# Kernel optimization log

Hardware: AMD Instinct MI355X
Metric: run time of the kernel (lower is better)

Reference implementation:

```python
import jax, jax.numpy as jnp
import numpy as np

B, C, O, H, W, K, PAD = 8, 256, 256, 56, 56, 3, 1
KK = K * K


def setup_inputs() -> dict:
    key = jax.random.key(0)
    k1, k2, k3, k4 = jax.random.split(key, 4)
    x = jax.random.normal(k1, (B, C, H, W), jnp.float32)
    # offset conv params (original zero-inits; small random used so sampling is off-grid)
    w_off = jax.random.normal(k2, (2 * KK, C, K, K), jnp.float32) * 0.01
    b_off = jnp.zeros((2 * KK,), jnp.float32)
    # deformable conv weight/bias (torchvision DeformConv2d default has bias)
    w_dcn = jax.random.normal(k3, (O, C, K, K), jnp.float32) * (1.0 / np.sqrt(C * KK))
    b_dcn = jax.random.normal(k4, (O,), jnp.float32) * 0.01
    return dict(x=x, w_off=w_off, b_off=b_off, w_dcn=w_dcn, b_dcn=b_dcn)


def _conv3x3(x, w, b):
    y = jax.lax.conv_general_dilated(
        x, w, window_strides=(1, 1), padding=((PAD, PAD), (PAD, PAD)),
        dimension_numbers=('NCHW', 'OIHW', 'NCHW'))
    return y + b[None, :, None, None]


def _deform_sample(x, py, px):
    """Zero-padded bilinear gather of x[B,C,H,W] at (py,px)[B,KK,H,W] -> [B,C,KK,H,W]."""
    xf = x.reshape(B, C, H * W)
    y0 = jnp.floor(py)
    x0 = jnp.floor(px)
    fy = py - y0
    fx = px - x0
    val = 0.0
    for dy, dx, wgt in ((0, 0, (1 - fy) * (1 - fx)),
                        (0, 1, (1 - fy) * fx),
                        (1, 0, fy * (1 - fx)),
                        (1, 1, fy * fx)):
        yc = y0 + dy
        xc = x0 + dx
        ok = (yc >= 0) & (yc < H) & (xc >= 0) & (xc < W)  # zero-padding outside
        yi = jnp.clip(yc, 0, H - 1).astype(jnp.int32)
        xi = jnp.clip(xc, 0, W - 1).astype(jnp.int32)
        idx = (yi * W + xi).reshape(B, 1, KK * H * W)  # broadcast over channel dim
        g = jnp.take_along_axis(xf, idx, axis=2).reshape(B, C, KK, H, W)
        val = val + (wgt * ok)[:, None] * g
    return val


def reference(x, w_off, b_off, w_dcn, b_dcn):
    # 1) predict per-pixel offsets: [B, 2*K*K, H, W], torchvision layout (dy,dx) pairs
    off = _conv3x3(x, w_off, b_off)
    dy = off[:, 0::2]  # [B, KK, H, W]
    dx = off[:, 1::2]
    # 2) sampling grid: base pixel + kernel tap offset + learned offset
    ky = (jnp.arange(KK) // K - PAD).astype(jnp.float32)
    kx = (jnp.arange(KK) % K - PAD).astype(jnp.float32)
    hgrid = jnp.arange(H, dtype=jnp.float32)
    wgrid = jnp.arange(W, dtype=jnp.float32)
    py = hgrid[None, None, :, None] + ky[None, :, None, None] + dy
    px = wgrid[None, None, None, :] + kx[None, :, None, None] + dx
    # 3) bilinear gather + weighted accumulation over (c, kernel tap)
    val = _deform_sample(x, py, px)  # [B, C, KK, H, W]
    out = jnp.einsum('bckhw,ock->bohw', val, w_dcn.reshape(O, C, KK))
    return out + b_dcn[None, :, None, None]
```

## Files before the change

### kernel.cpp

```cpp
#include <hip/hip_runtime.h>

#define B_  8
#define C_  256
#define O_  256
#define H_  56
#define W_  56
#define HW_ 3136
#define KK_ 9
#define CK_ 2304
#define NKC 72

typedef __bf16    bf16x8 __attribute__((ext_vector_type(8)));
typedef float     f32x4  __attribute__((ext_vector_type(4)));

__device__ __forceinline__ int swz4(int r) { return (r & 3) ^ ((r >> 2) & 3); }

__device__ __forceinline__ float blo(unsigned u) {
    return __builtin_bit_cast(float, u << 16);
}
__device__ __forceinline__ float bhi(unsigned u) {
    return __builtin_bit_cast(float, u & 0xffff0000u);
}
__device__ __forceinline__ unsigned pkbf(float lo, float hi) {
    unsigned short a = __builtin_bit_cast(unsigned short, (__bf16)lo);
    unsigned short b = __builtin_bit_cast(unsigned short, (__bf16)hi);
    return (unsigned)a | ((unsigned)b << 16);
}

__device__ __forceinline__ uint4 bilin4(uint4 c00, uint4 c01, uint4 c10, uint4 c11,
                                        float4 wg) {
    uint4 o;
    float lo_, hi_;
    lo_ = wg.x*blo(c00.x) + wg.y*blo(c01.x) + wg.z*blo(c10.x) + wg.w*blo(c11.x);
    hi_ = wg.x*bhi(c00.x) + wg.y*bhi(c01.x) + wg.z*bhi(c10.x) + wg.w*bhi(c11.x);
    o.x = pkbf(lo_, hi_);
    lo_ = wg.x*blo(c00.y) + wg.y*blo(c01.y) + wg.z*blo(c10.y) + wg.w*blo(c11.y);
    hi_ = wg.x*bhi(c00.y) + wg.y*bhi(c01.y) + wg.z*bhi(c10.y) + wg.w*bhi(c11.y);
    o.y = pkbf(lo_, hi_);
    lo_ = wg.x*blo(c00.z) + wg.y*blo(c01.z) + wg.z*blo(c10.z) + wg.w*blo(c11.z);
    hi_ = wg.x*bhi(c00.z) + wg.y*bhi(c01.z) + wg.z*bhi(c10.z) + wg.w*bhi(c11.z);
    o.z = pkbf(lo_, hi_);
    lo_ = wg.x*blo(c00.w) + wg.y*blo(c01.w) + wg.z*blo(c10.w) + wg.w*blo(c11.w);
    hi_ = wg.x*bhi(c00.w) + wg.y*bhi(c01.w) + wg.z*bhi(c10.w) + wg.w*bhi(c11.w);
    o.w = pkbf(lo_, hi_);
    return o;
}

__global__ __launch_bounds__(256) void k_buildA(const float* __restrict__ w,
                                                unsigned short* __restrict__ wA) {
    int d  = blockIdx.x * 256 + threadIdx.x;
    int kc = d >> 13;
    int rd = d & 8191;
    int m  = rd >> 5;
    int pos = rd & 31;
    int q  = (pos >> 3) ^ swz4(m);
    int kl = q * 8 + (pos & 7);
    int gk = kc * 32 + kl;
    int tap = gk >> 8, c = gk & 255;
    __bf16 v = (__bf16)w[m * CK_ + c * KK_ + tap];
    wA[d] = __builtin_bit_cast(unsigned short, v);
}

__global__ __launch_bounds__(256) void k_transx(const float* __restrict__ x,
                                                unsigned short* __restrict__ xT) {
    __shared__ float s[64][65];
    int bt   = blockIdx.x;
    int c64  = bt & 3;
    int hw64 = (bt >> 2) % 49;
    int b    = bt / 196;
    int tx = threadIdx.x & 63;
    int ty = threadIdx.x >> 6;
#pragma unroll
    for (int i = 0; i < 16; ++i)
        s[i * 4 + ty][tx] =
            x[((size_t)(b * 256 + c64 * 64 + i * 4 + ty)) * HW_ + hw64 * 64 + tx];
    __syncthreads();
#pragma unroll
    for (int i = 0; i < 16; ++i) {
        float v = s[tx][i * 4 + ty];
        xT[((size_t)b * HW_ + hw64 * 64 + i * 4 + ty) * 256 + c64 * 64 + tx] =
            __builtin_bit_cast(unsigned short, (__bf16)v);
    }
}

__global__ __launch_bounds__(512) void k_offc1(const float* __restrict__ x,
                                               const float* __restrict__ w_off,
                                               float* __restrict__ part) {
    __shared__ float partial[8][64][18];
    int t  = threadIdx.x;
    int p  = t & 63;
    int cg = __builtin_amdgcn_readfirstlane(t >> 6);
    int orig = blockIdx.x;
    int blk  = (orig & 7) * 196 + (orig >> 3);
    int sl   = blk & 3;
    int un   = blk >> 2;
    int b    = un / 49;
    int pos0 = (un % 49) * 64;
    int pos  = pos0 + p;
    int h = pos / W_;
    int w = pos % W_;
    const float* xb = x + (size_t)b * C_ * HW_;

    float acc[18];
#pragma unroll
    for (int i = 0; i < 18; ++i) acc[i] = 0.f;

    for (int cc = 0; cc < 8; ++cc) {
        int c = sl * 64 + cg * 8 + cc;
        const float* xp = xb + c * HW_;
        float v[9];
#pragma unroll
        for (int dh = -1; dh <= 1; ++dh)
#pragma unroll
            for (int dw = -1; dw <= 1; ++dw) {
                int hh = h + dh, ww = w + dw;
                bool ok = (hh >= 0) & (hh < H_) & (ww >= 0) & (ww < W_);
                v[(dh + 1) * 3 + dw + 1] = ok ? xp[hh * W_ + ww] : 0.f;
            }
        const float* wc = w_off + c * KK_;
#pragma unroll
        for (int oc = 0; oc < 18; ++oc) {
            const float* wr = wc + oc * CK_;
#pragma unroll
            for (int k = 0; k < KK_; ++k)
                acc[oc] = fmaf(v[k], wr[k], acc[oc]);
        }
    }
#pragma unroll
    for (int oc = 0; oc < 18; ++oc) partial[cg][p][oc] = acc[oc];
    __syncthreads();

    float* po = part + (size_t)sl * (B_ * 18 * HW_);
    for (int e = t; e < 64 * 18; e += 512) {
        int oc = e >> 6;
        int pp = e & 63;
        float s = 0.f;
#pragma unroll
        for (int g = 0; g < 8; ++g) s += partial[g][pp][oc];
        po[((size_t)b * 18 + oc) * HW_ + pos0 + pp] = s;
    }
}

__global__ __launch_bounds__(256) void k_offc2(const float* __restrict__ part,
                                               const float* __restrict__ b_off,
                                               float* __restrict__ off) {
    int i = blockIdx.x * 256 + threadIdx.x;
    const int NP = B_ * 18 * HW_;
    int oc = (i / HW_) % 18;
    off[i] = part[i] + part[i + NP] + part[i + 2 * NP] + part[i + 3 * NP]
           + b_off[oc];
}

template<bool ISSUEC, bool ISSUEA, bool PROD, bool RELID, bool RELWG>
__device__ __forceinline__ void fstage(
    int s, int chNext,
    const char* xb, const char* gA0,
    __bf16 (*s_b)[2048],
    int (*s_id)[64][4], float (*s_w)[64][4],
    int4& id, float4& wg,
    uint4 (&cUse)[4], uint4 (&cFill)[4],
    bf16x8 (&afUse)[4], bf16x8 (&afFill)[4],
    int aoffBase,
    int n, int tc, int sc, int lid, int quad, int swz,
    f32x4 (&acc)[4][4]) {

    if (RELID) {
        id = *(const int4*)s_id[(s + 2) >> 3][n];
    }
    if (RELWG) {
        wg = *(const float4*)s_w[(s + 1) >> 3][n];
    }
    if (ISSUEC) {
        const char* p = xb + chNext * 64 + tc * 16;
        cFill[0] = *(const uint4*)(p + id.x);
        cFill[1] = *(const uint4*)(p + id.y);
        cFill[2] = *(const uint4*)(p + id.z);
        cFill[3] = *(const uint4*)(p + id.w);
    }
    if (ISSUEA) {
        const char* ga = gA0 + (size_t)(s + 1) * 16384 + aoffBase;
        afFill[0] = *(const bf16x8*)(ga);
        afFill[1] = *(const bf16x8*)(ga + 1024);
        afFill[2] = *(const bf16x8*)(ga + 2048);
        afFill[3] = *(const bf16x8*)(ga + 3072);
    }

    const bf16x8* pb = (const bf16x8*)s_b[s & 1];
    bf16x8 bv[4];
#pragma unroll
    for (int ni = 0; ni < 4; ++ni)
        bv[ni] = pb[(ni * 16 + lid) * 4 + (quad ^ swz)];

    __builtin_amdgcn_s_setprio(1);
#pragma unroll
    for (int mi = 0; mi < 4; ++mi)
#pragma unroll
        for (int ni = 0; ni < 4; ++ni)
            acc[mi][ni] = __builtin_amdgcn_mfma_f32_16x16x32_bf16(
                afUse[mi], bv[ni], acc[mi][ni], 0, 0, 0);
    __builtin_amdgcn_s_setprio(0);

    if (PROD) {
        uint4 o = bilin4(cUse[0], cUse[1], cUse[2], cUse[3], wg);
        *(uint4*)((char*)s_b[(s & 1) ^ 1] + n * 64 + sc * 16) = o;
    }
    asm volatile("s_waitcnt lgkmcnt(0)" ::: "memory");
    __builtin_amdgcn_s_barrier();
    __builtin_amdgcn_sched_barrier(0);
}

__global__ __launch_bounds__(256, 3) void k_fused(
    const unsigned short* __restrict__ xT,
    const float* __restrict__ off,
    const __bf16* __restrict__ wA,
    const float* __restrict__ b_dcn,
    float* __restrict__ out) {

    __shared__ __bf16 s_b[2][2048];
    __shared__ int    s_id[KK_][64][4];
    __shared__ float  s_w [KK_][64][4];

    int bid  = blockIdx.x;
    int g    = (bid & 7) * 49 + (bid >> 3);
    int b    = g / 49;
    int pos0 = (g % 49) * 64;
    int t    = threadIdx.x;
    int lane = t & 63;
    int wv   = t >> 6;
    int lid  = lane & 15;
    int quad = lane >> 4;
    int swz  = swz4(lid);

    for (int e = t; e < KK_ * 64; e += 256) {
        int k = e >> 6, n = e & 63;
        int pos = pos0 + n;
        int h = pos / W_, w = pos % W_;
        float dy = off[((size_t)b * 18 + 2 * k) * HW_ + pos];
        float dx = off[((size_t)b * 18 + 2 * k + 1) * HW_ + pos];
        float py = (float)(h + k / 3 - 1) + dy;
        float px = (float)(w + k % 3 - 1) + dx;
        float y0f = floorf(py), x0f = floorf(px);
        float fy = py - y0f, fx = px - x0f;
        int y0 = (int)y0f, x0 = (int)x0f;
        int y1 = y0 + 1,   x1 = x0 + 1;
        float oy0 = (y0 >= 0 && y0 < H_) ? 1.f : 0.f;
        float oy1 = (y1 >= 0 && y1 < H_) ? 1.f : 0.f;
        float ox0 = (x0 >= 0 && x0 < W_) ? 1.f : 0.f;
        float ox1 = (x1 >= 0 && x1 < W_) ? 1.f : 0.f;
        int y0c = min(max(y0, 0), H_ - 1), y1c = min(max(y1, 0), H_ - 1);
        int x0c = min(max(x0, 0), W_ - 1), x1c = min(max(x1, 0), W_ - 1);
        s_id[k][n][0] = (y0c * W_ + x0c) * 512;
        s_id[k][n][1] = (y0c * W_ + x1c) * 512;
        s_id[k][n][2] = (y1c * W_ + x0c) * 512;
        s_id[k][n][3] = (y1c * W_ + x1c) * 512;
        s_w[k][n][0] = (1.f - fy) * (1.f - fx) * oy0 * ox0;
        s_w[k][n][1] = (1.f - fy) * fx         * oy0 * ox1;
        s_w[k][n][2] = fy * (1.f - fx)         * oy1 * ox0;
        s_w[k][n][3] = fy * fx                 * oy1 * ox1;
    }
    __syncthreads();

    int n  = t >> 2;
    int tc = t & 3;
    int sc = tc ^ swz4(n);
    const char* xb  = (const char*)(xT + (size_t)b * HW_ * 256);
    const char* gA0 = (const char*)wA;
    int aoffBase = (wv * 64 + lid) * 64 + (quad ^ swz) * 16;

    f32x4 acc[4][4];
#pragma unroll
    for (int mi = 0; mi < 4; ++mi)
#pragma unroll
        for (int ni = 0; ni < 4; ++ni)
            acc[mi][ni] = (f32x4)(0.f);

    int4   id = *(const int4*)s_id[0][n];
    float4 wg = *(const float4*)s_w[0][n];
    uint4  cA[4], cB[4];
    bf16x8 afA[4], afB[4];

    {
        const char* p0 = xb + tc * 16;
        uint4 c0[4];
        c0[0] = *(const uint4*)(p0 + id.x);
        c0[1] = *(const uint4*)(p0 + id.y);
        c0[2] = *(const uint4*)(p0 + id.z);
        c0[3] = *(const uint4*)(p0 + id.w);
        const char* ga = gA0 + aoffBase;
        afA[0] = *(const bf16x8*)(ga);
        afA[1] = *(const bf16x8*)(ga + 1024);
        afA[2] = *(const bf16x8*)(ga + 2048);
        afA[3] = *(const bf16x8*)(ga + 3072);
        const char* p1 = xb + 64 + tc * 16;
        cA[0] = *(const uint4*)(p1 + id.x);
        cA[1] = *(const uint4*)(p1 + id.y);
        cA[2] = *(const uint4*)(p1 + id.z);
        cA[3] = *(const uint4*)(p1 + id.w);
        uint4 o = bilin4(c0[0], c0[1], c0[2], c0[3], wg);
        *(uint4*)((char*)s_b[0] + n * 64 + sc * 16) = o;
    }
    asm volatile("s_waitcnt lgkmcnt(0)" ::: "memory");
    __builtin_amdgcn_s_barrier();
    __builtin_amdgcn_sched_barrier(0);

    for (int tap = 0; tap < 8; ++tap) {
        int s0 = tap * 8;
        fstage<true, true, true, false, false>(s0 + 0, 2, xb, gA0, s_b, s_id, s_w, id, wg, cA, cB, afA, afB, aoffBase, n, tc, sc, lid, quad, swz, acc);
        fstage<true, true, true, false, false>(s0 + 1, 3, xb, gA0, s_b, s_id, s_w, id, wg, cB, cA, afB, afA, aoffBase, n, tc, sc, lid, quad, swz, acc);
        fstage<true, true, true, false, false>(s0 + 2, 4, xb, gA0, s_b, s_id, s_w, id, wg, cA, cB, afA, afB, aoffBase, n, tc, sc, lid, quad, swz, acc);
        fstage<true, true, true, false, false>(s0 + 3, 5, xb, gA0, s_b, s_id, s_w, id, wg, cB, cA, afB, afA, aoffBase, n, tc, sc, lid, quad, swz, acc);
        fstage<true, true, true, false, false>(s0 + 4, 6, xb, gA0, s_b, s_id, s_w, id, wg, cA, cB, afA, afB, aoffBase, n, tc, sc, lid, quad, swz, acc);
        fstage<true, true, true, false, false>(s0 + 5, 7, xb, gA0, s_b, s_id, s_w, id, wg, cB, cA, afB, afA, aoffBase, n, tc, sc, lid, quad, swz, acc);
        fstage<true, true, true, true,  false>(s0 + 6, 0, xb, gA0, s_b, s_id, s_w, id, wg, cA, cB, afA, afB, aoffBase, n, tc, sc, lid, quad, swz, acc);
        fstage<true, true, true, false, true >(s0 + 7, 1, xb, gA0, s_b, s_id, s_w, id, wg, cB, cA, afB, afA, aoffBase, n, tc, sc, lid, quad, swz, acc);
    }
    fstage<true,  true,  true,  false, false>(64, 2, xb, gA0, s_b, s_id, s_w, id, wg, cA, cB, afA, afB, aoffBase, n, tc, sc, lid, quad, swz, acc);
    fstage<true,  true,  true,  false, false>(65, 3, xb, gA0, s_b, s_id, s_w, id, wg, cB, cA, afB, afA, aoffBase, n, tc, sc, lid, quad, swz, acc);
    fstage<true,  true,  true,  false, false>(66, 4, xb, gA0, s_b, s_id, s_w, id, wg, cA, cB, afA, afB, aoffBase, n, tc, sc, lid, quad, swz, acc);
    fstage<true,  true,  true,  false, false>(67, 5, xb, gA0, s_b, s_id, s_w, id, wg, cB, cA, afB, afA, aoffBase, n, tc, sc, lid, quad, swz, acc);
    fstage<true,  true,  true,  false, false>(68, 6, xb, gA0, s_b, s_id, s_w, id, wg, cA, cB, afA, afB, aoffBase, n, tc, sc, lid, quad, swz, acc);
    fstage<true,  true,  true,  false, false>(69, 7, xb, gA0, s_b, s_id, s_w, id, wg, cB, cA, afB, afA, aoffBase, n, tc, sc, lid, quad, swz, acc);
    fstage<false, true,  true,  false, false>(70, 0, xb, gA0, s_b, s_id, s_w, id, wg, cA, cB, afA, afB, aoffBase, n, tc, sc, lid, quad, swz, acc);
    fstage<false, false, false, false, false>(71, 1, xb, gA0, s_b, s_id, s_w, id, wg, cB, cA, afB, afA, aoffBase, n, tc, sc, lid, quad, swz, acc);

#pragma unroll
    for (int mi = 0; mi < 4; ++mi) {
#pragma unroll
        for (int r = 0; r < 4; ++r) {
            int m = wv * 64 + mi * 16 + quad * 4 + r;
            float bias = b_dcn[m];
            float* po = out + ((size_t)b * O_ + m) * HW_ + pos0 + lid;
#pragma unroll
            for (int ni = 0; ni < 4; ++ni)
                po[ni * 16] = acc[mi][ni][r] + bias;
        }
    }
}

extern "C" void kernel_launch(void* const* d_in, const int* in_sizes, int n_in,
                              void* d_out, int out_size, void* d_ws, size_t ws_size,
                              hipStream_t stream) {
    const float* x     = (const float*)d_in[0];
    const float* w_off = (const float*)d_in[1];
    const float* b_off = (const float*)d_in[2];
    const float* w_dcn = (const float*)d_in[3];
    const float* b_dcn = (const float*)d_in[4];
    float* out = (float*)d_out;

    const size_t offBytes  = (size_t)451584 * 4;
    const size_t wABytes   = (size_t)589824 * 2;
    const size_t xTBytes   = (size_t)B_ * HW_ * 256 * 2;
    float*          off  = (float*)d_ws;
    unsigned short* wA   = (unsigned short*)((char*)d_ws + offBytes);
    unsigned short* xT   = (unsigned short*)((char*)d_ws + offBytes + wABytes);
    float*          part = (float*)((char*)d_ws + offBytes + wABytes + xTBytes);

    k_buildA <<<2304, 256, 0, stream>>>(w_dcn, wA);
    k_transx <<<1568, 256, 0, stream>>>(x, xT);
    k_offc1  <<<1568, 512, 0, stream>>>(x, w_off, part);
    k_offc2  <<<1764, 256, 0, stream>>>(part, b_off, off);
    k_fused  <<<392,  256, 0, stream>>>(xT, off, (const __bf16*)wA, b_dcn, out);
}
```

Baseline: 217.6 us.

## Shorten x-gather prefetch depth to one stage and relax occupancy bound

```diff
diff --git a/kernel.cpp b/kernel.cpp
--- a/kernel.cpp
+++ b/kernel.cpp
@@ -151,31 +151,29 @@
            + b_off[oc];
 }
 
-template<bool ISSUEC, bool ISSUEA, bool PROD, bool RELID, bool RELWG>
+template<bool ISSUEC, bool ISSUEA, bool PROD, bool RELOAD>
 __device__ __forceinline__ void fstage(
     int s, int chNext,
     const char* xb, const char* gA0,
     __bf16 (*s_b)[2048],
     int (*s_id)[64][4], float (*s_w)[64][4],
     int4& id, float4& wg,
-    uint4 (&cUse)[4], uint4 (&cFill)[4],
     bf16x8 (&afUse)[4], bf16x8 (&afFill)[4],
     int aoffBase,
     int n, int tc, int sc, int lid, int quad, int swz,
     f32x4 (&acc)[4][4]) {
 
-    if (RELID) {
-        id = *(const int4*)s_id[(s + 2) >> 3][n];
-    }
-    if (RELWG) {
+    if (RELOAD) {
+        id = *(const int4*)s_id[(s + 1) >> 3][n];
         wg = *(const float4*)s_w[(s + 1) >> 3][n];
     }
+    uint4 c0, c1, c2, c3;
     if (ISSUEC) {
         const char* p = xb + chNext * 64 + tc * 16;
-        cFill[0] = *(const uint4*)(p + id.x);
-        cFill[1] = *(const uint4*)(p + id.y);
-        cFill[2] = *(const uint4*)(p + id.z);
-        cFill[3] = *(const uint4*)(p + id.w);
+        c0 = *(const uint4*)(p + id.x);
+        c1 = *(const uint4*)(p + id.y);
+        c2 = *(const uint4*)(p + id.z);
+        c3 = *(const uint4*)(p + id.w);
     }
     if (ISSUEA) {
         const char* ga = gA0 + (size_t)(s + 1) * 16384 + aoffBase;
@@ -201,7 +199,7 @@
     __builtin_amdgcn_s_setprio(0);
 
     if (PROD) {
-        uint4 o = bilin4(cUse[0], cUse[1], cUse[2], cUse[3], wg);
+        uint4 o = bilin4(c0, c1, c2, c3, wg);
         *(uint4*)((char*)s_b[(s & 1) ^ 1] + n * 64 + sc * 16) = o;
     }
     asm volatile("s_waitcnt lgkmcnt(0)" ::: "memory");
@@ -209,7 +207,7 @@
     __builtin_amdgcn_sched_barrier(0);
 }
 
-__global__ __launch_bounds__(256, 3) void k_fused(
+__global__ __launch_bounds__(256, 2) void k_fused(
     const unsigned short* __restrict__ xT,
     const float* __restrict__ off,
     const __bf16* __restrict__ wA,
@@ -276,27 +274,20 @@
 
     int4   id = *(const int4*)s_id[0][n];
     float4 wg = *(const float4*)s_w[0][n];
-    uint4  cA[4], cB[4];
     bf16x8 afA[4], afB[4];
 
     {
         const char* p0 = xb + tc * 16;
-        uint4 c0[4];
-        c0[0] = *(const uint4*)(p0 + id.x);
-        c0[1] = *(const uint4*)(p0 + id.y);
-        c0[2] = *(const uint4*)(p0 + id.z);
-        c0[3] = *(const uint4*)(p0 + id.w);
+        uint4 c0 = *(const uint4*)(p0 + id.x);
+        uint4 c1 = *(const uint4*)(p0 + id.y);
+        uint4 c2 = *(const uint4*)(p0 + id.z);
+        uint4 c3 = *(const uint4*)(p0 + id.w);
         const char* ga = gA0 + aoffBase;
         afA[0] = *(const bf16x8*)(ga);
         afA[1] = *(const bf16x8*)(ga + 1024);
         afA[2] = *(const bf16x8*)(ga + 2048);
         afA[3] = *(const bf16x8*)(ga + 3072);
-        const char* p1 = xb + 64 + tc * 16;
-        cA[0] = *(const uint4*)(p1 + id.x);
-        cA[1] = *(const uint4*)(p1 + id.y);
-        cA[2] = *(const uint4*)(p1 + id.z);
-        cA[3] = *(const uint4*)(p1 + id.w);
-        uint4 o = bilin4(c0[0], c0[1], c0[2], c0[3], wg);
+        uint4 o = bilin4(c0, c1, c2, c3, wg);
         *(uint4*)((char*)s_b[0] + n * 64 + sc * 16) = o;
     }
     asm volatile("s_waitcnt lgkmcnt(0)" ::: "memory");
@@ -305,23 +296,23 @@
 
     for (int tap = 0; tap < 8; ++tap) {
         int s0 = tap * 8;
-        fstage<true, true, true, false, false>(s0 + 0, 2, xb, gA0, s_b, s_id, s_w, id, wg, cA, cB, afA, afB, aoffBase, n, tc, sc, lid, quad, swz, acc);
-        fstage<true, true, true, false, false>(s0 + 1, 3, xb, gA0, s_b, s_id, s_w, id, wg, cB, cA, afB, afA, aoffBase, n, tc, sc, lid, quad, swz, acc);
-        fstage<true, true, true, false, false>(s0 + 2, 4, xb, gA0, s_b, s_id, s_w, id, wg, cA, cB, afA, afB, aoffBase, n, tc, sc, lid, quad, swz, acc);
-        fstage<true, true, true, false, false>(s0 + 3, 5, xb, gA0, s_b, s_id, s_w, id, wg, cB, cA, afB, afA, aoffBase, n, tc, sc, lid, quad, swz, acc);
-        fstage<true, true, true, false, false>(s0 + 4, 6, xb, gA0, s_b, s_id, s_w, id, wg, cA, cB, afA, afB, aoffBase, n, tc, sc, lid, quad, swz, acc);
-        fstage<true, true, true, false, false>(s0 + 5, 7, xb, gA0, s_b, s_id, s_w, id, wg, cB, cA, afB, afA, aoffBase, n, tc, sc, lid, quad, swz, acc);
-        fstage<true, true, true, true,  false>(s0 + 6, 0, xb, gA0, s_b, s_id, s_w, id, wg, cA, cB, afA, afB, aoffBase, n, tc, sc, lid, quad, swz, acc);
-        fstage<true, true, true, false, true >(s0 + 7, 1, xb, gA0, s_b, s_id, s_w, id, wg, cB, cA, afB, afA, aoffBase, n, tc, sc, lid, quad, swz, acc);
-    }
-    fstage<true,  true,  true,  false, false>(64, 2, xb, gA0, s_b, s_id, s_w, id, wg, cA, cB, afA, afB, aoffBase, n, tc, sc, lid, quad, swz, acc);
-    fstage<true,  true,  true,  false, false>(65, 3, xb, gA0, s_b, s_id, s_w, id, wg, cB, cA, afB, afA, aoffBase, n, tc, sc, lid, quad, swz, acc);
-    fstage<true,  true,  true,  false, false>(66, 4, xb, gA0, s_b, s_id, s_w, id, wg, cA, cB, afA, afB, aoffBase, n, tc, sc, lid, quad, swz, acc);
-    fstage<true,  true,  true,  false, false>(67, 5, xb, gA0, s_b, s_id, s_w, id, wg, cB, cA, afB, afA, aoffBase, n, tc, sc, lid, quad, swz, acc);
-    fstage<true,  true,  true,  false, false>(68, 6, xb, gA0, s_b, s_id, s_w, id, wg, cA, cB, afA, afB, aoffBase, n, tc, sc, lid, quad, swz, acc);
-    fstage<true,  true,  true,  false, false>(69, 7, xb, gA0, s_b, s_id, s_w, id, wg, cB, cA, afB, afA, aoffBase, n, tc, sc, lid, quad, swz, acc);
-    fstage<false, true,  true,  false, false>(70, 0, xb, gA0, s_b, s_id, s_w, id, wg, cA, cB, afA, afB, aoffBase, n, tc, sc, lid, quad, swz, acc);
-    fstage<false, false, false, false, false>(71, 1, xb, gA0, s_b, s_id, s_w, id, wg, cB, cA, afB, afA, aoffBase, n, tc, sc, lid, quad, swz, acc);
+        fstage<true, true, true, false>(s0 + 0, 1, xb, gA0, s_b, s_id, s_w, id, wg, afA, afB, aoffBase, n, tc, sc, lid, quad, swz, acc);
+        fstage<true, true, true, false>(s0 + 1, 2, xb, gA0, s_b, s_id, s_w, id, wg, afB, afA, aoffBase, n, tc, sc, lid, quad, swz, acc);
+        fstage<true, true, true, false>(s0 + 2, 3, xb, gA0, s_b, s_id, s_w, id, wg, afA, afB, aoffBase, n, tc, sc, lid, quad, swz, acc);
+        fstage<true, true, true, false>(s0 + 3, 4, xb, gA0, s_b, s_id, s_w, id, wg, afB, afA, aoffBase, n, tc, sc, lid, quad, swz, acc);
+        fstage<true, true, true, false>(s0 + 4, 5, xb, gA0, s_b, s_id, s_w, id, wg, afA, afB, aoffBase, n, tc, sc, lid, quad, swz, acc);
+        fstage<true, true, true, false>(s0 + 5, 6, xb, gA0, s_b, s_id, s_w, id, wg, afB, afA, aoffBase, n, tc, sc, lid, quad, swz, acc);
+        fstage<true, true, true, false>(s0 + 6, 7, xb, gA0, s_b, s_id, s_w, id, wg, afA, afB, aoffBase, n, tc, sc, lid, quad, swz, acc);
+        fstage<true, true, true, true >(s0 + 7, 0, xb, gA0, s_b, s_id, s_w, id, wg, afB, afA, aoffBase, n, tc, sc, lid, quad, swz, acc);
+    }
+    fstage<true,  true,  true,  false>(64, 1, xb, gA0, s_b, s_id, s_w, id, wg, afA, afB, aoffBase, n, tc, sc, lid, quad, swz, acc);
+    fstage<true,  true,  true,  false>(65, 2, xb, gA0, s_b, s_id, s_w, id, wg, afB, afA, aoffBase, n, tc, sc, lid, quad, swz, acc);
+    fstage<true,  true,  true,  false>(66, 3, xb, gA0, s_b, s_id, s_w, id, wg, afA, afB, aoffBase, n, tc, sc, lid, quad, swz, acc);
+    fstage<true,  true,  true,  false>(67, 4, xb, gA0, s_b, s_id, s_w, id, wg, afB, afA, aoffBase, n, tc, sc, lid, quad, swz, acc);
+    fstage<true,  true,  true,  false>(68, 5, xb, gA0, s_b, s_id, s_w, id, wg, afA, afB, aoffBase, n, tc, sc, lid, quad, swz, acc);
+    fstage<true,  true,  true,  false>(69, 6, xb, gA0, s_b, s_id, s_w, id, wg, afB, afA, aoffBase, n, tc, sc, lid, quad, swz, acc);
+    fstage<true,  true,  true,  false>(70, 7, xb, gA0, s_b, s_id, s_w, id, wg, afA, afB, aoffBase, n, tc, sc, lid, quad, swz, acc);
+    fstage<false, false, false, false>(71, 0, xb, gA0, s_b, s_id, s_w, id, wg, afB, afA, aoffBase, n, tc, sc, lid, quad, swz, acc);
 
 #pragma unroll
     for (int mi = 0; mi < 4; ++mi) {
```

New measurement: 193.8 us. -10.9%, faster.
